# Kernel tuning notes

Measured on AMD Instinct MI355X. Metric: run time of the kernel, lower is better.

Reference implementation:

```python
import jax, jax.numpy as jnp
import numpy as np

B, N, T, C = 1, 50000, 12, 2   # t must equal pred_num=12, c=in_dim=2
E = 1_600_000                  # ~32 avg degree
DMK = 16


def setup_inputs() -> dict:
    key = jax.random.key(0)
    ks = jax.random.split(key, 13)
    s = 0.1
    x = jax.random.normal(ks[0], (B, N, T, C), dtype=jnp.float32)
    edge_index = jax.random.randint(ks[1], (2, E), 0, B * N, dtype=jnp.int64)
    # GRU(in=2, hidden=1): torch packs gates as [r, z, n]
    W_ih = jax.random.normal(ks[2], (3, C)) * s
    W_hh = jax.random.normal(ks[3], (3, 1)) * s
    b_ih = jax.random.normal(ks[4], (3,)) * s
    b_hh = jax.random.normal(ks[5], (3,)) * s
    # GATConv(24 -> 12, heads=1)
    gat_W = jax.random.normal(ks[6], (T * C, T)) * s
    a_src = jax.random.normal(ks[7], (T,)) * s
    a_dst = jax.random.normal(ks[8], (T,)) * s
    gat_b = jax.random.normal(ks[9], (T,)) * s
    gamma = jax.random.normal(ks[10], (T,))
    lin_W = jax.random.normal(ks[11], (T, DMK)) * s
    lin_b = jax.random.normal(ks[12], (DMK,)) * s
    return dict(x=x, edge_index=edge_index, W_ih=W_ih, W_hh=W_hh, b_ih=b_ih,
                b_hh=b_hh, gat_W=gat_W, a_src=a_src, a_dst=a_dst, gat_b=gat_b,
                gamma=gamma, lin_W=lin_W, lin_b=lin_b)


def reference(x, edge_index, W_ih, W_hh, b_ih, b_hh, gat_W, a_src, a_dst,
              gat_b, gamma, lin_W, lin_b):
    b, n, t, c = x.shape
    BN = b * n

    # --- GRU branch: torch nn.GRU is seq-first, so the recurrence runs over
    # the b*n axis with an effective batch of t (faithful to the source).
    x_seq = x.reshape(BN, t, c)  # (seq=BN, batch=t, feat=c)

    def step(h, xt):
        gi = xt @ W_ih.T + b_ih          # (t, 3)
        gh = h @ W_hh.T + b_hh           # (t, 3)
        r = jax.nn.sigmoid(gi[:, 0:1] + gh[:, 0:1])
        z = jax.nn.sigmoid(gi[:, 1:2] + gh[:, 1:2])
        nn_ = jnp.tanh(gi[:, 2:3] + r * gh[:, 2:3])
        h_new = (1.0 - z) * nn_ + z * h  # (t, 1)
        return h_new, h_new

    h0 = jnp.zeros((t, 1), x.dtype)
    _, hs = jax.lax.scan(step, h0, x_seq)  # (BN, t, 1)
    x_gru = hs[..., 0]                     # (BN, t)

    # --- GAT branch (PyG GATConv defaults: heads=1, self-loops, lrelu 0.2)
    xp = x.reshape(BN, t * c) @ gat_W      # (BN, t)
    loops = jnp.arange(BN, dtype=edge_index.dtype)
    src = jnp.concatenate([edge_index[0], loops])
    dst = jnp.concatenate([edge_index[1], loops])
    asrc = xp @ a_src                      # (BN,)
    adst = xp @ a_dst
    e = jax.nn.leaky_relu(asrc[src] + adst[dst], 0.2)
    m = jax.lax.stop_gradient(jax.ops.segment_max(e, dst, num_segments=BN))
    ex = jnp.exp(e - m[dst])
    denom = jax.ops.segment_sum(ex, dst, num_segments=BN)
    coef = ex / (denom[dst] + 1e-16)
    x_gat = jax.ops.segment_sum(coef[:, None] * xp[src], dst,
                                num_segments=BN) + gat_b  # (BN, t)

    # --- sigmoid-gated fusion + output linear
    x_mk = jax.nn.sigmoid(gamma) * x_gat + jax.nn.sigmoid(1.0 - gamma) * x_gru
    out = x_mk @ lin_W + lin_b             # (BN, d_mk)
    return out.reshape(b, n, -1)
```

## Files before the change

### kernel.cpp

```cpp
#include <hip/hip_runtime.h>
#include <hip/hip_bf16.h>

#define T_DIM 12
#define C_DIM 2
#define DMK_DIM 16

#define GRU_CHUNKS 8192
#define GRU_WARM 40
#define GRU_BLOCKS 192

#define NPB 64
#define NPB_SHIFT 6
#define NBUCK_MAX 1024
#define BUCKET_CAP 2432
#define BIN_THREADS 512
#define BIN_EPT 16
#define BIN_CHUNK (BIN_THREADS * BIN_EPT)
#define CSLOT 40
#define CROW 256
#define XP_PAD 16

__device__ __forceinline__ float sigmoid_fast(float x) {
    return 1.f / (1.f + __expf(-x));
}

__global__ void __launch_bounds__(512)
fused_k1(const float* __restrict__ x, int n_nodes,
         const int* __restrict__ ei, int n_edges, int nb_bin, int capb,
         const float* __restrict__ W_ih,
         const float* __restrict__ W_hh,
         const float* __restrict__ b_ih,
         const float* __restrict__ b_hh,
         const float* __restrict__ gat_W,
         const float* __restrict__ a_src,
         const float* __restrict__ a_dst,
         float* __restrict__ xgru,
         float* __restrict__ xp,
         float* __restrict__ adst,
         unsigned* __restrict__ Cmat,
         unsigned* __restrict__ bfile)
{
    __shared__ __align__(16) char smem[4096 + 4096 + 32 + 32768];

    if (blockIdx.x < (unsigned)nb_bin) {
        unsigned* lcnt    = (unsigned*)smem;
        unsigned* seg2    = lcnt + NBUCK_MAX;
        unsigned* wtot    = seg2 + NBUCK_MAX;
        unsigned* sortbuf = wtot + 8;

        int tid  = threadIdx.x;
        int chunk = blockIdx.x;
        int base = chunk * BIN_CHUNK;
        int nvalid = min(BIN_CHUNK, n_edges - base);
        for (int i = tid; i < NBUCK_MAX; i += BIN_THREADS) lcnt[i] = 0;
        __syncthreads();

        unsigned pk[BIN_EPT], rr[BIN_EPT];
#pragma unroll
        for (int k = 0; k < BIN_EPT; ++k) {
            int e = base + k * BIN_THREADS + tid;
            if (e < n_edges) {
                unsigned s = (unsigned)ei[e];
                unsigned d = (unsigned)ei[n_edges + e];
                unsigned b = d >> NPB_SHIFT;
                pk[k] = s | ((d & (NPB - 1)) << 16) | (b << 22);
                rr[k] = atomicAdd(&lcnt[b], 1u);
            } else pk[k] = 0xffffffffu;
        }
        __syncthreads();

        for (int i = tid; i < NBUCK_MAX; i += BIN_THREADS)
            Cmat[(size_t)i * CROW + chunk] = min(lcnt[i], (unsigned)CSLOT);

        unsigned a0 = lcnt[2 * tid], a1 = lcnt[2 * tid + 1];
        unsigned v  = a0 + a1;
        unsigned inc = v;
#pragma unroll
        for (int off = 1; off < 64; off <<= 1) {
            unsigned u = __shfl_up(inc, off, 64);
            if ((tid & 63) >= off) inc += u;
        }
        if ((tid & 63) == 63) wtot[tid >> 6] = inc;
        __syncthreads();
        if (tid < 8) {
            unsigned w = wtot[tid];
            unsigned winc = w;
#pragma unroll
            for (int off = 1; off < 8; off <<= 1) {
                unsigned u = __shfl_up(winc, off, 8);
                if (tid >= off) winc += u;
            }
            wtot[tid] = winc - w;
        }
        __syncthreads();
        unsigned ex = inc - v + wtot[tid >> 6];
        seg2[2 * tid]     = ex;
        seg2[2 * tid + 1] = ex + a0;
        __syncthreads();

#pragma unroll
        for (int k = 0; k < BIN_EPT; ++k) {
            if (pk[k] == 0xffffffffu) continue;
            sortbuf[seg2[pk[k] >> 22] + rr[k]] = pk[k];
        }
        __syncthreads();

        unsigned cbase = (unsigned)chunk * CSLOT;
        for (int j = tid; j < nvalid; j += BIN_THREADS) {
            unsigned p = sortbuf[j];
            unsigned b = p >> 22;
            unsigned r = (unsigned)j - seg2[b];
            if (r < CSLOT)
                bfile[(size_t)b * capb + cbase + r] = p;
        }
        return;
    }

    if (blockIdx.x < (unsigned)(nb_bin + GRU_BLOCKS)) {
        int tid   = (blockIdx.x - nb_bin) * 512 + threadIdx.x;
        int chunk = tid / T_DIM;
        int t     = tid - chunk * T_DIM;
        int L     = (n_nodes + GRU_CHUNKS - 1) / GRU_CHUNKS;
        int start = chunk * L;
        if (start >= n_nodes) return;
        int end = min(start + L, n_nodes);
        int s0  = max(start - GRU_WARM, 0);
        int sm  = end - 1;

        float wi_r0 = W_ih[0], wi_r1 = W_ih[1];
        float wi_z0 = W_ih[2], wi_z1 = W_ih[3];
        float wi_n0 = W_ih[4], wi_n1 = W_ih[5];
        float wh_r = W_hh[0], wh_z = W_hh[1], wh_n = W_hh[2];
        float br   = b_ih[0] + b_hh[0];
        float bz   = b_ih[1] + b_hh[1];
        float bin_ = b_ih[2];
        float bhn  = b_hh[2];

        const float2* xf = reinterpret_cast<const float2*>(x);
        float h = 0.f;

#define GRU_STEP(q, sj)                                                     \
        {                                                                   \
            float gr = fmaf(q.x, wi_r0, fmaf(q.y, wi_r1, fmaf(h, wh_r, br)));\
            float gz = fmaf(q.x, wi_z0, fmaf(q.y, wi_z1, fmaf(h, wh_z, bz)));\
            float r_ = sigmoid_fast(gr);                                    \
            float z_ = sigmoid_fast(gz);                                    \
            float gn = fmaf(q.x, wi_n0, fmaf(q.y, wi_n1, bin_))             \
                     + r_ * fmaf(h, wh_n, bhn);                             \
            float e2 = __expf(2.f * gn);                                    \
            float th = 1.f - 2.f / (e2 + 1.f);                              \
            h = (1.f - z_) * th + z_ * h;                                   \
            if ((sj) >= start && (sj) < end) xgru[(sj) * T_DIM + t] = h;    \
        }

        for (int s = s0; s < end; s += 8) {
            float2 q0 = xf[(size_t)min(s + 0, sm) * T_DIM + t];
            float2 q1 = xf[(size_t)min(s + 1, sm) * T_DIM + t];
            float2 q2 = xf[(size_t)min(s + 2, sm) * T_DIM + t];
            float2 q3 = xf[(size_t)min(s + 3, sm) * T_DIM + t];
            float2 q4 = xf[(size_t)min(s + 4, sm) * T_DIM + t];
            float2 q5 = xf[(size_t)min(s + 5, sm) * T_DIM + t];
            float2 q6 = xf[(size_t)min(s + 6, sm) * T_DIM + t];
            float2 q7 = xf[(size_t)min(s + 7, sm) * T_DIM + t];
            GRU_STEP(q0, s + 0); GRU_STEP(q1, s + 1);
            GRU_STEP(q2, s + 2); GRU_STEP(q3, s + 3);
            GRU_STEP(q4, s + 4); GRU_STEP(q5, s + 5);
            GRU_STEP(q6, s + 6); GRU_STEP(q7, s + 7);
        }
#undef GRU_STEP
        return;
    }

    float* sW = (float*)smem;
    float* sa = sW + 24 * T_DIM;
    float* sd = sa + T_DIM;
    for (int i = threadIdx.x; i < 24 * T_DIM; i += 512) sW[i] = gat_W[i];
    if (threadIdx.x < T_DIM) {
        sa[threadIdx.x] = a_src[threadIdx.x];
        sd[threadIdx.x] = a_dst[threadIdx.x];
    }
    __syncthreads();

    int i = (blockIdx.x - nb_bin - GRU_BLOCKS) * 512 + threadIdx.x;
    if (i >= n_nodes) return;

    float xi[24];
    const float4* xv = reinterpret_cast<const float4*>(x + (size_t)i * 24);
#pragma unroll
    for (int q = 0; q < 6; ++q) {
        float4 v = xv[q];
        xi[4 * q + 0] = v.x; xi[4 * q + 1] = v.y;
        xi[4 * q + 2] = v.z; xi[4 * q + 3] = v.w;
    }

    float p[T_DIM];
    float as = 0.f, ad = 0.f;
#pragma unroll
    for (int j = 0; j < T_DIM; ++j) {
        float s = 0.f;
#pragma unroll
        for (int k = 0; k < 24; ++k) s = fmaf(xi[k], sW[k * T_DIM + j], s);
        p[j] = s;
        as = fmaf(s, sa[j], as);
        ad = fmaf(s, sd[j], ad);
    }

    float4* xpo = reinterpret_cast<float4*>(xp + (size_t)i * XP_PAD);
    xpo[0] = make_float4(p[0], p[1],  p[2],  as);
    xpo[1] = make_float4(p[3], p[4],  p[5],  as);
    xpo[2] = make_float4(p[6], p[7],  p[8],  as);
    xpo[3] = make_float4(p[9], p[10], p[11], as);
    adst[i] = ad;
}

__global__ void __launch_bounds__(512)
bucket_final(const unsigned* __restrict__ Cmat,
             const unsigned* __restrict__ bfile,
             const float* __restrict__ xp,
             const float* __restrict__ adst,
             const float* __restrict__ xgru,
             const float* __restrict__ gat_b,
             const float* __restrict__ gamma,
             const float* __restrict__ lin_W,
             const float* __restrict__ lin_b,
             float* __restrict__ out, int n_nodes, int nb_bin, int capb)
{
    __shared__ unsigned lsort[BUCKET_CAP];
    __shared__ float accbuf[128 * 16];
    __shared__ unsigned scnt[CROW];
    __shared__ float sadst[NPB];
    __shared__ int   hist[NPB];
    __shared__ int   seg[NPB + 1];
    __shared__ float sW[T_DIM * DMK_DIM];
    __shared__ float sgb[T_DIM], sg1[T_DIM], sg2[T_DIM], slb[DMK_DIM];

    int tid = threadIdx.x;
    int b = blockIdx.x;
    int base = b * NPB;
    int nloc = min(NPB, n_nodes - base);
    int nslots = nb_bin * CSLOT;
    const unsigned* bf = bfile + (size_t)b * capb;

    if (tid < NPB) {
        hist[tid] = 0;
        sadst[tid] = (tid < nloc) ? adst[base + tid] : 0.f;
    }
    for (int i = tid; i < nb_bin; i += 512) scnt[i] = Cmat[(size_t)b * CROW + i];
    for (int i = tid; i < T_DIM * DMK_DIM; i += 512) sW[i] = lin_W[i];
    if (tid < T_DIM) {
        float g = gamma[tid];
        sgb[tid] = gat_b[tid];
        sg1[tid] = sigmoid_fast(g);
        sg2[tid] = sigmoid_fast(1.f - g);
    }
    if (tid < DMK_DIM) slb[tid] = lin_b[tid];
    __syncthreads();

    for (int s = tid; s < nslots; s += 512) {
        int c = s / CSLOT;
        int j = s - c * CSLOT;
        if ((unsigned)j < scnt[c]) {
            unsigned p = bf[s];
            atomicAdd(&hist[(p >> 16) & (NPB - 1)], 1);
        }
    }
    __syncthreads();

    if (tid < NPB) {
        int v = hist[tid];
        int inc = v;
#pragma unroll
        for (int off = 1; off < NPB; off <<= 1) {
            int t = __shfl_up(inc, off, 64);
            if (tid >= off) inc += t;
        }
        seg[tid] = inc - v;
        if (tid == NPB - 1) seg[NPB] = inc;
    }
    __syncthreads();
    if (tid < NPB) hist[tid] = 0;
    __syncthreads();

    for (int s = tid; s < nslots; s += 512) {
        int c = s / CSLOT;
        int j = s - c * CSLOT;
        if ((unsigned)j < scnt[c]) {
            unsigned p = bf[s];
            int l = (p >> 16) & (NPB - 1);
            int r = atomicAdd(&hist[l], 1);
            int pos = seg[l] + r;
            if (pos < BUCKET_CAP) lsort[pos] = p;
        }
    }
    __syncthreads();

    int g    = tid >> 2;
    int c    = tid & 3;
    int l    = g & (NPB - 1);
    int half = g >> NPB_SHIFT;
    int sbeg = seg[l] + half;
    int s1   = min(seg[l + 1], BUCKET_CAP);
    float adl = sadst[l];

    float3 vacc = make_float3(0.f, 0.f, 0.f);
    float  wsum = 0.f;

    int len = s1 - sbeg;
    int m   = (len > 0) ? ((len + 1) >> 1) : 0;

#define LOADXP(r) (*reinterpret_cast<const float4*>(                         \
        xp + (size_t)((r) & 0xFFFFu) * XP_PAD + c * 4))

    if (m > 0) {
        int mc = m - 1;
        unsigned r0 = lsort[sbeg];
        unsigned r1 = lsort[sbeg + 2 * min(1, mc)];
        unsigned r2 = lsort[sbeg + 2 * min(2, mc)];
        unsigned r3 = lsort[sbeg + 2 * min(3, mc)];
        float4 v0 = LOADXP(r0);
        float4 v1 = LOADXP(r1);
        float4 v2 = LOADXP(r2);
        float4 v3 = LOADXP(r3);

        int m4 = (m + 3) & ~3;
        for (int i = 0; i < m4; i += 4) {
            {
                float ev = v0.w + adl;
                ev = ev >= 0.f ? ev : 0.2f * ev;
                float w = __expf(ev);
                vacc.x = fmaf(w, v0.x, vacc.x);
                vacc.y = fmaf(w, v0.y, vacc.y);
                vacc.z = fmaf(w, v0.z, vacc.z);
                wsum += w;
                int nx = i + 4;
                if (nx < m) { r0 = lsort[sbeg + 2 * nx]; v0 = LOADXP(r0); }
            }
            {
                float ev = v1.w + adl;
                ev = ev >= 0.f ? ev : 0.2f * ev;
                float w = (i + 1 < m) ? __expf(ev) : 0.f;
                vacc.x = fmaf(w, v1.x, vacc.x);
                vacc.y = fmaf(w, v1.y, vacc.y);
                vacc.z = fmaf(w, v1.z, vacc.z);
                wsum += w;
                int nx = i + 5;
                if (nx < m) { r1 = lsort[sbeg + 2 * nx]; v1 = LOADXP(r1); }
            }
            {
                float ev = v2.w + adl;
                ev = ev >= 0.f ? ev : 0.2f * ev;
                float w = (i + 2 < m) ? __expf(ev) : 0.f;
                vacc.x = fmaf(w, v2.x, vacc.x);
                vacc.y = fmaf(w, v2.y, vacc.y);
                vacc.z = fmaf(w, v2.z, vacc.z);
                wsum += w;
                int nx = i + 6;
                if (nx < m) { r2 = lsort[sbeg + 2 * nx]; v2 = LOADXP(r2); }
            }
            {
                float ev = v3.w + adl;
                ev = ev >= 0.f ? ev : 0.2f * ev;
                float w = (i + 3 < m) ? __expf(ev) : 0.f;
                vacc.x = fmaf(w, v3.x, vacc.x);
                vacc.y = fmaf(w, v3.y, vacc.y);
                vacc.z = fmaf(w, v3.z, vacc.z);
                wsum += w;
                int nx = i + 7;
                if (nx < m) { r3 = lsort[sbeg + 2 * nx]; v3 = LOADXP(r3); }
            }
        }
    }
#undef LOADXP

    float4* ab = reinterpret_cast<float4*>(accbuf + g * 16 + c * 4);
    *ab = make_float4(vacc.x, vacc.y, vacc.z, wsum);
    __syncthreads();

    if (tid < nloc) {
        int i = base + tid;
        const float4* psi = reinterpret_cast<const float4*>(
            xp + (size_t)i * XP_PAD);
        float4 q0 = psi[0], q1 = psi[1], q2 = psi[2], q3 = psi[3];

        float ev = q0.w + sadst[tid];
        ev = ev >= 0.f ? ev : 0.2f * ev;
        float w = __expf(ev);

        const float* a0 = accbuf + tid * 16;
        const float* a1 = accbuf + (tid + 64) * 16;
        float den = a0[3] + a1[3] + w + 1e-16f;
        float inv = 1.f / den;

        float av[T_DIM] = {
            fmaf(w, q0.x, a0[0]  + a1[0]),
            fmaf(w, q0.y, a0[1]  + a1[1]),
            fmaf(w, q0.z, a0[2]  + a1[2]),
            fmaf(w, q1.x, a0[4]  + a1[4]),
            fmaf(w, q1.y, a0[5]  + a1[5]),
            fmaf(w, q1.z, a0[6]  + a1[6]),
            fmaf(w, q2.x, a0[8]  + a1[8]),
            fmaf(w, q2.y, a0[9]  + a1[9]),
            fmaf(w, q2.z, a0[10] + a1[10]),
            fmaf(w, q3.x, a0[12] + a1[12]),
            fmaf(w, q3.y, a0[13] + a1[13]),
            fmaf(w, q3.z, a0[14] + a1[14])
        };

        const float* gri = xgru + (size_t)i * T_DIM;
        float mk[T_DIM];
#pragma unroll
        for (int j = 0; j < T_DIM; ++j) {
            float gat = fmaf(av[j], inv, sgb[j]);
            mk[j] = sg1[j] * gat + sg2[j] * gri[j];
        }

        float o[DMK_DIM];
#pragma unroll
        for (int j = 0; j < DMK_DIM; ++j) o[j] = slb[j];
#pragma unroll
        for (int k = 0; k < T_DIM; ++k) {
#pragma unroll
            for (int j = 0; j < DMK_DIM; ++j)
                o[j] = fmaf(mk[k], sW[k * DMK_DIM + j], o[j]);
        }

        float4* po = reinterpret_cast<float4*>(out + (size_t)i * DMK_DIM);
#pragma unroll
        for (int q = 0; q < 4; ++q)
            po[q] = make_float4(o[4*q+0], o[4*q+1], o[4*q+2], o[4*q+3]);
    }
}

extern "C" void kernel_launch(void* const* d_in, const int* in_sizes, int n_in,
                              void* d_out, int out_size, void* d_ws, size_t ws_size,
                              hipStream_t stream)
{
    const float* x      = (const float*)d_in[0];
    const int*   ei     = (const int*)d_in[1];
    const float* W_ih   = (const float*)d_in[2];
    const float* W_hh   = (const float*)d_in[3];
    const float* b_ih   = (const float*)d_in[4];
    const float* b_hh   = (const float*)d_in[5];
    const float* gat_W  = (const float*)d_in[6];
    const float* a_src  = (const float*)d_in[7];
    const float* a_dst  = (const float*)d_in[8];
    const float* gat_b  = (const float*)d_in[9];
    const float* gamma  = (const float*)d_in[10];
    const float* lin_W  = (const float*)d_in[11];
    const float* lin_b  = (const float*)d_in[12];
    float* out = (float*)d_out;

    int n_nodes = in_sizes[0] / (T_DIM * C_DIM);
    int n_edges = in_sizes[1] / 2;
    int nbuck   = (n_nodes + NPB - 1) / NPB;
    int nb_bin  = (n_edges + BIN_CHUNK - 1) / BIN_CHUNK;
    int capb    = nb_bin * CSLOT;

    char* ws = (char*)d_ws;
    size_t off = 0;
    auto alloc = [&](size_t bytes) {
        void* p = ws + off;
        off = (off + bytes + 15) & ~(size_t)15;
        return p;
    };
    float*    xp    = (float*)alloc((size_t)n_nodes * XP_PAD * 4);
    float*    xgru  = (float*)alloc((size_t)n_nodes * T_DIM * 4);
    float*    adst  = (float*)alloc((size_t)n_nodes * 4);
    unsigned* Cmat  = (unsigned*)alloc((size_t)NBUCK_MAX * CROW * 4);
    unsigned* bfile = (unsigned*)alloc((size_t)nbuck * capb * 4);

    int node_blocks = (n_nodes + 511) / 512;
    fused_k1<<<nb_bin + GRU_BLOCKS + node_blocks, 512, 0, stream>>>(
        x, n_nodes, ei, n_edges, nb_bin, capb, W_ih, W_hh, b_ih, b_hh,
        gat_W, a_src, a_dst, xgru, xp, adst, Cmat, bfile);

    bucket_final<<<nbuck, 512, 0, stream>>>(
        Cmat, bfile, xp, adst, xgru,
        gat_b, gamma, lin_W, lin_b, out, n_nodes, nb_bin, capb);
}
```

Measured before the change: 49.07 us.

## Transpose count matrix and compact bucket slots via prefix scan in final kernel

Stores the per-chunk bucket counts chunk-major, so the binning writes are coalesced, and bucket_final reads a strided column instead. In bucket_final, an exclusive scan over the per-chunk counts plus a binary search gathers only the valid records. Each record is read from global memory once and held in registers, where before two passes each scanned every slot. The first atomic rank is reused for the placement, so the second histogram pass goes away. It adds register pressure, fixes per-thread capacity at 5 records (2560 per bucket), and makes the count reads in the final kernel strided.

After: 43.59 us, median of 2. 11.2% less time.

```diff
diff --git a/kernel.cpp b/kernel.cpp
--- a/kernel.cpp
+++ b/kernel.cpp
@@ -70,7 +70,7 @@
         __syncthreads();
 
         for (int i = tid; i < NBUCK_MAX; i += BIN_THREADS)
-            Cmat[(size_t)i * CROW + chunk] = min(lcnt[i], (unsigned)CSLOT);
+            Cmat[(size_t)chunk * NBUCK_MAX + i] = min(lcnt[i], (unsigned)CSLOT);
 
         unsigned a0 = lcnt[2 * tid], a1 = lcnt[2 * tid + 1];
         unsigned v  = a0 + a1;
@@ -228,6 +228,8 @@
     __shared__ unsigned lsort[BUCKET_CAP];
     __shared__ float accbuf[128 * 16];
     __shared__ unsigned scnt[CROW];
+    __shared__ unsigned cellOff[CROW + 1];
+    __shared__ unsigned wq[4];
     __shared__ float sadst[NPB];
     __shared__ int   hist[NPB];
     __shared__ int   seg[NPB + 1];
@@ -238,14 +240,14 @@
     int b = blockIdx.x;
     int base = b * NPB;
     int nloc = min(NPB, n_nodes - base);
-    int nslots = nb_bin * CSLOT;
     const unsigned* bf = bfile + (size_t)b * capb;
 
     if (tid < NPB) {
         hist[tid] = 0;
         sadst[tid] = (tid < nloc) ? adst[base + tid] : 0.f;
     }
-    for (int i = tid; i < nb_bin; i += 512) scnt[i] = Cmat[(size_t)b * CROW + i];
+    for (int i = tid; i < CROW; i += 512)
+        scnt[i] = (i < nb_bin) ? Cmat[(size_t)i * NBUCK_MAX + b] : 0u;
     for (int i = tid; i < T_DIM * DMK_DIM; i += 512) sW[i] = lin_W[i];
     if (tid < T_DIM) {
         float g = gamma[tid];
@@ -256,12 +258,55 @@
     if (tid < DMK_DIM) slb[tid] = lin_b[tid];
     __syncthreads();
 
-    for (int s = tid; s < nslots; s += 512) {
-        int c = s / CSLOT;
-        int j = s - c * CSLOT;
-        if ((unsigned)j < scnt[c]) {
-            unsigned p = bf[s];
-            atomicAdd(&hist[(p >> 16) & (NPB - 1)], 1);
+    if (tid < CROW) {
+        unsigned v = scnt[tid];
+        unsigned inc = v;
+#pragma unroll
+        for (int off = 1; off < 64; off <<= 1) {
+            unsigned u = __shfl_up(inc, off, 64);
+            if ((tid & 63) >= off) inc += u;
+        }
+        if ((tid & 63) == 63) wq[tid >> 6] = inc;
+        __syncthreads();
+        if (tid < 4) {
+            unsigned w = wq[tid];
+            unsigned winc = w;
+#pragma unroll
+            for (int off = 1; off < 4; off <<= 1) {
+                unsigned u = __shfl_up(winc, off, 4);
+                if (tid >= off) winc += u;
+            }
+            wq[tid] = winc - w;
+        }
+        __syncthreads();
+        unsigned ex = inc - v + wq[tid >> 6];
+        cellOff[tid] = ex;
+        if (tid == CROW - 1) cellOff[CROW] = ex + v;
+    } else {
+        __syncthreads();
+        __syncthreads();
+    }
+    __syncthreads();
+
+    int count = (int)cellOff[CROW];
+
+    unsigned rec[5];
+    int rk[5];
+    int nk = 0;
+#pragma unroll
+    for (int k = 0; k < 5; ++k) {
+        int gidx = tid + k * 512;
+        if (gidx < count) {
+            int lo = 0, hi = CROW;
+#pragma unroll
+            for (int it = 0; it < 8; ++it) {
+                int mid = (lo + hi) >> 1;
+                if (cellOff[mid] <= (unsigned)gidx) lo = mid; else hi = mid;
+            }
+            int j = gidx - (int)cellOff[lo];
+            rec[k] = bf[lo * CSLOT + j];
+            rk[k] = atomicAdd(&hist[(rec[k] >> 16) & (NPB - 1)], 1);
+            nk = k + 1;
         }
     }
     __syncthreads();
@@ -278,18 +323,11 @@
         if (tid == NPB - 1) seg[NPB] = inc;
     }
     __syncthreads();
-    if (tid < NPB) hist[tid] = 0;
-    __syncthreads();
-
-    for (int s = tid; s < nslots; s += 512) {
-        int c = s / CSLOT;
-        int j = s - c * CSLOT;
-        if ((unsigned)j < scnt[c]) {
-            unsigned p = bf[s];
-            int l = (p >> 16) & (NPB - 1);
-            int r = atomicAdd(&hist[l], 1);
-            int pos = seg[l] + r;
-            if (pos < BUCKET_CAP) lsort[pos] = p;
+#pragma unroll
+    for (int k = 0; k < 5; ++k) {
+        if (k < nk) {
+            int pos = seg[(rec[k] >> 16) & (NPB - 1)] + rk[k];
+            if (pos < BUCKET_CAP) lsort[pos] = rec[k];
         }
     }
     __syncthreads();
@@ -466,7 +504,7 @@
     float*    xp    = (float*)alloc((size_t)n_nodes * XP_PAD * 4);
     float*    xgru  = (float*)alloc((size_t)n_nodes * T_DIM * 4);
     float*    adst  = (float*)alloc((size_t)n_nodes * 4);
-    unsigned* Cmat  = (unsigned*)alloc((size_t)NBUCK_MAX * CROW * 4);
+    unsigned* Cmat  = (unsigned*)alloc((size_t)CROW * NBUCK_MAX * 4);
     unsigned* bfile = (unsigned*)alloc((size_t)nbuck * capb * 4);
 
     int node_blocks = (n_nodes + 511) / 512;
```
